# Performance work log

Hardware: AMD Instinct MI355X
Metric: run time of the kernel (lower is better)

Reference implementation:

```python
import jax, jax.numpy as jnp
import numpy as np

N = 50_000          # num_nodes
E = 800_000         # num_edges (avg degree 16)
DIMS = [512, 256, 256, 7]   # embedding_dim
SCALING = 2.0


def _glorot(key, shape):
    lim = float(np.sqrt(6.0 / (shape[0] + shape[1])))
    return jax.random.uniform(key, shape, jnp.float32, -lim, lim)


def setup_inputs() -> dict:
    key = jax.random.key(0)
    ks = jax.random.split(key, 16)
    inp = {
        "x": jax.random.normal(ks[0], (N, DIMS[0]), jnp.float32),
        "edge_index": jax.random.randint(ks[1], (2, E), 0, N, dtype=jnp.int32),
        # GCNConv weights (3 layers)
        "W1": _glorot(ks[2], (DIMS[0], DIMS[1])), "b1": jnp.zeros((DIMS[1],), jnp.float32),
        "W2": _glorot(ks[3], (DIMS[1], DIMS[2])), "b2": jnp.zeros((DIMS[2],), jnp.float32),
        "W3": _glorot(ks[4], (DIMS[2], DIMS[3])), "b3": jnp.zeros((DIMS[3],), jnp.float32),
        # pseudo_mlp: Linear(512,512) -> ReLU -> Linear(512,64) -> ReLU -> Linear(64,out)
        "mw1": _glorot(ks[5], (DIMS[0], 512)), "mb1": jnp.zeros((512,), jnp.float32),
        "mw2": _glorot(ks[6], (512, 64)),      "mb2": jnp.zeros((64,), jnp.float32),
        "mw3": _glorot(ks[7], (64, DIMS[-1])), "mb3": jnp.zeros((DIMS[-1],), jnp.float32),
        # parsing_mats[0] (only index 0 is used: learn_soft_edge3 always called with ln=0)
        "parsing0": jnp.ones((DIMS[-1], DIMS[-1]), jnp.float32) / SCALING,
    }
    return inp


def _gcn_conv(h_in, row, col, edge_weight, W, b):
    """PyG-style GCNConv with self-loops, symmetric norm, and per-edge weights."""
    h = h_in @ W                                  # [N, out]
    loop = jnp.arange(N, dtype=row.dtype)
    r = jnp.concatenate([row, loop])
    c = jnp.concatenate([col, loop])
    ew = jnp.concatenate([edge_weight, jnp.ones((N,), h.dtype)])
    deg = jax.ops.segment_sum(ew, c, num_segments=N)
    dinv = jnp.where(deg > 0, jax.lax.rsqrt(jnp.maximum(deg, 1e-12)), 0.0)
    norm = dinv[r] * ew * dinv[c]                 # [E+N]
    out = jax.ops.segment_sum(h[r] * norm[:, None], c, num_segments=N)
    return out + b


def _learn_soft_edge(x, row, col, mw1, mb1, mw2, mb2, mw3, mb3, parsing0):
    # pseudo_mlp logits
    h = jax.nn.relu(x @ mw1 + mb1)
    h = jax.nn.relu(h @ mw2 + mb2)
    logits = h @ mw3 + mb3                        # [N, C]
    s = logits[row]                               # start_logits [E, C]
    e = logits[col]                               # end_logits   [E, C]
    parsing = jax.nn.relu(SCALING * parsing0)     # [C, C]
    # diag(bmm(outer(s,e), P)).sum(-1) == sum_{c,d} s[e,c] * e[e,d] * P[d,c]
    ew = jnp.sum(s * (e @ parsing), axis=1)       # [E]
    mean = ew.mean()
    var = ew.var(ddof=1)                          # torch .var() is unbiased
    return (ew - mean) * jnp.sqrt(1e-4 / var) + 1.0


def reference(x, edge_index, W1, b1, W2, b2, W3, b3,
              mw1, mb1, mw2, mb2, mw3, mb3, parsing0):
    row, col = edge_index[0], edge_index[1]
    ew = _learn_soft_edge(x, row, col, mw1, mb1, mw2, mb2, mw3, mb3, parsing0)
    # layer 0
    h0 = _gcn_conv(x, row, col, ew, W1, b1)       # h = x (saved, pre-ReLU)
    x1 = jax.nn.relu(h0)                          # dropout is identity in eval
    # layer 1 (+ residual to h0)
    x2 = _gcn_conv(x1, row, col, ew, W2, b2)
    x2 = jax.nn.relu(x2) + h0
    # layer 2 (final, no activation)
    out = _gcn_conv(x2, row, col, ew, W3, b3)     # [N, n_classes]
    return out
```

## Files before the change

### kernel.cpp

```cpp
#include <hip/hip_runtime.h>

#define NN 50000
#define EE 800000
#define NB_EDGE 3125
#define NB_E1   1563
#define NB_SCAN 196

typedef __attribute__((ext_vector_type(4))) float f32x4;
typedef __attribute__((ext_vector_type(8))) short bf16x8;
typedef __attribute__((ext_vector_type(8))) unsigned short u16x8;

typedef const __attribute__((address_space(1))) void* gas_p;
typedef __attribute__((address_space(3))) void* las_p;

__device__ __forceinline__ float bf2f(unsigned short u) {
  union { unsigned int i; float f; } v; v.i = ((unsigned int)u) << 16; return v.f;
}
__device__ __forceinline__ unsigned short f2bf(float f) {
  union { float f; unsigned int i; } v; v.f = f;
  unsigned int u = v.i;
  return (unsigned short)((u + 0x7FFFu + ((u >> 16) & 1u)) >> 16);
}

__device__ __forceinline__ int xcd_swizzle(int orig, int nwg) {
  int xcd = orig & 7;
  int pos = orig >> 3;
  int q = nwg >> 3, r = nwg & 7;
  return (xcd < r ? xcd * (q + 1) : r * (q + 1) + (xcd - r) * q) + pos;
}

constexpr size_t O_XBF  = 0;
constexpr size_t O_H1   = O_XBF + 51200000;
constexpr size_t O_G1   = O_H1  + 51200000;
constexpr size_t O_X1   = O_G1  + 25600000;
constexpr size_t O_H2   = O_X1  + 25600000;
constexpr size_t O_LG   = O_H2  + 6400000;
constexpr size_t O_TG   = O_LG  + 1600000;
constexpr size_t O_EWR  = O_TG  + 1600000;
constexpr size_t O_W3P  = O_EWR + 3200000;
constexpr size_t O_CSR  = O_W3P + 3200000;
constexpr size_t O_MW1T = O_CSR + 6400000;
constexpr size_t O_W1T  = O_MW1T + 524288;
constexpr size_t O_W2T  = O_W1T  + 262144;
constexpr size_t O_MW2T = O_W2T  + 131072;
constexpr size_t O_DEG  = O_MW2T + 65536;
constexpr size_t O_CNT  = O_DEG  + 200192;
constexpr size_t O_CUR  = O_CNT  + 200192;
constexpr size_t O_RED  = O_CUR  + 200192;
constexpr size_t O_RPT  = O_RED  + 256;
constexpr size_t O_DINV = O_RPT  + 200192;
constexpr size_t O_BSUM = O_DINV + 200192;

__global__ __launch_bounds__(256) void conv_f2bf4(const float* __restrict__ in,
                                                  unsigned short* __restrict__ out, int n4) {
  int i = blockIdx.x * 256 + threadIdx.x;
  if (i >= n4) return;
  const float4 v = ((const float4*)in)[i];
  ushort4 o; o.x = f2bf(v.x); o.y = f2bf(v.y); o.z = f2bf(v.z); o.w = f2bf(v.w);
  ((ushort4*)out)[i] = o;
}

__global__ __launch_bounds__(256)
void conv_weights(const float* __restrict__ mw1, const float* __restrict__ W1,
                  const float* __restrict__ W2, const float* __restrict__ mw2,
                  const float* __restrict__ W3,
                  unsigned short* __restrict__ mw1t, unsigned short* __restrict__ w1t,
                  unsigned short* __restrict__ w2t, unsigned short* __restrict__ mw2t,
                  float* __restrict__ w3p)
{
  int i = blockIdx.x * 256 + threadIdx.x;
  if (i < 262144) {
    int k = i >> 9, n = i & 511;
    mw1t[(size_t)n * 512 + k] = f2bf(mw1[i]);
  } else if (i < 393216) {
    int j = i - 262144, k = j >> 8, n = j & 255;
    w1t[(size_t)n * 512 + k] = f2bf(W1[j]);
  } else if (i < 458752) {
    int j = i - 393216, k = j >> 8, n = j & 255;
    w2t[(size_t)n * 256 + k] = f2bf(W2[j]);
  } else if (i < 491520) {
    int j = i - 458752, k = j >> 6, n = j & 63;
    mw2t[(size_t)n * 512 + k] = f2bf(mw2[j]);
  } else if (i < 493568) {
    int j = i - 491520, d = j >> 3, c = j & 7;
    w3p[j] = (c < 7) ? W3[d * 7 + c] : 0.f;
  }
}

#define GEMM_STAGE(buf, k0)                                                        \
  _Pragma("unroll")                                                                \
  for (int r = 0; r < 4; ++r) {                                                    \
    const int row = r * 32 + wid * 8 + srow8;                                      \
    int ga = bm + row; ga = ga < M_ ? ga : M_ - 1;                                 \
    int gb = bn + row; gb = gb < N_ ? gb : N_ - 1;                                 \
    __builtin_amdgcn_global_load_lds((gas_p)(pA_ + ((size_t)ga * lda_ + (k0)) * 2 + sks * 16), \
                                     (las_p)(ldsA[buf] + row * 64), 16, 0, 0);     \
    __builtin_amdgcn_global_load_lds((gas_p)(pB_ + ((size_t)gb * ldb_ + (k0)) * 2 + sks * 16), \
                                     (las_p)(ldsB[buf] + row * 64), 16, 0, 0);     \
  }

#define GEMM_BODY(A, lda, Bt, ldb_K, M, Ncols, K, bm, bn)                          \
  __shared__ unsigned short ldsA[2][128 * 64];                                     \
  __shared__ unsigned short ldsB[2][128 * 64];                                     \
  const char* pA_ = (const char*)(A);                                              \
  const char* pB_ = (const char*)(Bt);                                             \
  const int lda_ = (lda), ldb_ = (ldb_K), M_ = (M), N_ = (Ncols);                  \
  const int tid  = threadIdx.x;                                                    \
  const int lane = tid & 63;                                                       \
  const int wid  = tid >> 6;                                                       \
  const int wm   = (wid >> 1) << 6;                                                \
  const int wn   = (wid & 1) << 6;                                                 \
  f32x4 acc[4][4] = {};                                                            \
  const int srow8 = lane >> 3;                                                     \
  const int sks   = (lane & 7) ^ srow8;                                            \
  const int nt    = (K) >> 6;                                                      \
  GEMM_STAGE(0, 0)                                                                 \
  for (int t = 0; t < nt; ++t) {                                                   \
    const int cur = t & 1;                                                         \
    if (t + 1 < nt) {                                                              \
      GEMM_STAGE(cur ^ 1, (t + 1) << 6)                                            \
      asm volatile("s_waitcnt vmcnt(8)" ::: "memory");                             \
    } else {                                                                       \
      asm volatile("s_waitcnt vmcnt(0)" ::: "memory");                             \
    }                                                                              \
    __builtin_amdgcn_s_barrier();                                                  \
    __builtin_amdgcn_sched_barrier(0);                                             \
    const int q   = lane >> 4;                                                     \
    const int r15 = lane & 15;                                                     \
    _Pragma("unroll")                                                              \
    for (int kk = 0; kk < 2; ++kk) {                                               \
      bf16x8 af[4], bfr[4];                                                        \
      _Pragma("unroll")                                                            \
      for (int m = 0; m < 4; ++m) {                                                \
        const int ra = wm + m * 16 + r15;                                          \
        af[m]  = *(const bf16x8*)(ldsA[cur] + ra * 64 + (((kk << 2) + q) ^ (ra & 7)) * 8); \
        const int rb = wn + m * 16 + r15;                                          \
        bfr[m] = *(const bf16x8*)(ldsB[cur] + rb * 64 + (((kk << 2) + q) ^ (rb & 7)) * 8); \
      }                                                                            \
      _Pragma("unroll")                                                            \
      for (int m = 0; m < 4; ++m)                                                  \
        _Pragma("unroll")                                                          \
        for (int n = 0; n < 4; ++n)                                                \
          acc[m][n] = __builtin_amdgcn_mfma_f32_16x16x32_bf16(af[m], bfr[n], acc[m][n], 0, 0, 0); \
    }                                                                              \
    __builtin_amdgcn_sched_barrier(0);                                             \
    __builtin_amdgcn_s_barrier();                                                  \
  }

template<bool RELU, bool BIAS>
__global__ __launch_bounds__(256)
void gemm_bf16(const unsigned short* __restrict__ A, int lda,
               const unsigned short* __restrict__ Bt,
               const float* __restrict__ bias,
               unsigned short* __restrict__ C, int ldc,
               int M, int N, int K)
{
  const int nwg  = gridDim.x * gridDim.y;
  const int wgid = xcd_swizzle(blockIdx.y * gridDim.x + blockIdx.x, nwg);
  const int bn   = (wgid % gridDim.x) << 7;
  const int bm   = (wgid / gridDim.x) << 7;

  GEMM_BODY(A, lda, Bt, K, M, N, K, bm, bn)

  const int q   = lane >> 4;
  const int r15 = lane & 15;
#pragma unroll
  for (int m = 0; m < 4; ++m) {
#pragma unroll
    for (int n = 0; n < 4; ++n) {
      const int gc = bn + wn + n * 16 + r15;
#pragma unroll
      for (int i = 0; i < 4; ++i) {
        const int gr = bm + wm + m * 16 + q * 4 + i;
        if (gr < M && gc < N) {
          float f = acc[m][n][i];
          if (BIAS) f += bias[gc];
          if (RELU) f = fmaxf(f, 0.f);
          C[(size_t)gr * ldc + gc] = f2bf(f);
        }
      }
    }
  }
}

__global__ __launch_bounds__(256)
void gemm_fused(const unsigned short* __restrict__ A,
                const unsigned short* __restrict__ Bt,
                const float* __restrict__ mb1,
                unsigned short* __restrict__ h1,
                unsigned short* __restrict__ g1,
                int M)
{
  const int nwg  = gridDim.x * gridDim.y;
  const int wgid = xcd_swizzle(blockIdx.y * gridDim.x + blockIdx.x, nwg);
  const int bnt  = wgid % gridDim.x;
  const int bn   = bnt << 7;
  const int bm   = (wgid / gridDim.x) << 7;

  GEMM_BODY(A, 512, Bt, 512, M, 768, 512, bm, bn)

  const int q   = lane >> 4;
  const int r15 = lane & 15;
  if (bnt < 4) {
#pragma unroll
    for (int m = 0; m < 4; ++m) {
#pragma unroll
      for (int n = 0; n < 4; ++n) {
        const int gc = bn + wn + n * 16 + r15;
        const float b = mb1[gc];
#pragma unroll
        for (int i = 0; i < 4; ++i) {
          const int gr = bm + wm + m * 16 + q * 4 + i;
          if (gr < M) h1[(size_t)gr * 512 + gc] = f2bf(fmaxf(acc[m][n][i] + b, 0.f));
        }
      }
    }
  } else {
#pragma unroll
    for (int m = 0; m < 4; ++m) {
#pragma unroll
      for (int n = 0; n < 4; ++n) {
        const int gc = bn - 512 + wn + n * 16 + r15;
#pragma unroll
        for (int i = 0; i < 4; ++i) {
          const int gr = bm + wm + m * 16 + q * 4 + i;
          if (gr < M) g1[(size_t)gr * 256 + gc] = f2bf(acc[m][n][i]);
        }
      }
    }
  }
}

__global__ __launch_bounds__(256)
void logits_kernel(const unsigned short* __restrict__ h2, const float* __restrict__ mw3,
                   const float* __restrict__ mb3, const float* __restrict__ par,
                   float* __restrict__ Lg, float* __restrict__ Tg)
{
  __shared__ float w[64 * 8];
  __shared__ float P[64];
  int tid = threadIdx.x;
  for (int i = tid; i < 512; i += 256) {
    int k = i >> 3, c = i & 7;
    w[i] = (c < 7) ? mw3[k * 7 + c] : 0.f;
  }
  if (tid < 64) {
    int d = tid >> 3, c = tid & 7;
    P[tid] = (d < 7 && c < 7) ? fmaxf(2.0f * par[d * 7 + c], 0.f) : 0.f;
  }
  __syncthreads();
  int n = blockIdx.x * 256 + tid;
  if (n >= NN) return;
  const unsigned short* hr = h2 + (size_t)n * 64;
  f32x4 L0 = {0,0,0,0}, L1 = {0,0,0,0};
  for (int k = 0; k < 64; k += 4) {
    ushort4 v = *(const ushort4*)(hr + k);
    float xs[4] = {bf2f(v.x), bf2f(v.y), bf2f(v.z), bf2f(v.w)};
#pragma unroll
    for (int j = 0; j < 4; ++j) {
      L0 += xs[j] * *(const f32x4*)&w[(k + j) * 8];
      L1 += xs[j] * *(const f32x4*)&w[(k + j) * 8 + 4];
    }
  }
  float Ls[8] = {L0[0], L0[1], L0[2], L0[3], L1[0], L1[1], L1[2], 0.f};
#pragma unroll
  for (int c = 0; c < 7; ++c) Ls[c] += mb3[c];
  f32x4 T0 = {0,0,0,0}, T1 = {0,0,0,0};
#pragma unroll
  for (int d = 0; d < 7; ++d) {
    T0 += Ls[d] * *(const f32x4*)&P[d * 8];
    T1 += Ls[d] * *(const f32x4*)&P[d * 8 + 4];
  }
  f32x4 o0 = {Ls[0], Ls[1], Ls[2], Ls[3]};
  f32x4 o1 = {Ls[4], Ls[5], Ls[6], 0.f};
  *(f32x4*)(Lg + (size_t)n * 8)     = o0;
  *(f32x4*)(Lg + (size_t)n * 8 + 4) = o1;
  *(f32x4*)(Tg + (size_t)n * 8)     = T0;
  *(f32x4*)(Tg + (size_t)n * 8 + 4) = T1;
}

__global__ __launch_bounds__(256)
void edge1_kernel(const int* __restrict__ row, const int* __restrict__ col,
                  const float* __restrict__ Lg, const float* __restrict__ Tg,
                  float* __restrict__ ew_raw, int* __restrict__ cnt,
                  double* __restrict__ part)
{
  __shared__ double shs[4], shs2[4];
  const int e0 = blockIdx.x * 512 + threadIdx.x;
  const int e1 = e0 + 256;
  double s = 0.0, s2 = 0.0;
  if (e1 < EE) {
    int r0 = row[e0], c0 = col[e0];
    int r1 = row[e1], c1 = col[e1];
    float4 a00 = *(const float4*)(Lg + (size_t)r0 * 8);
    float4 a01 = *(const float4*)(Lg + (size_t)r0 * 8 + 4);
    float4 a10 = *(const float4*)(Lg + (size_t)r1 * 8);
    float4 a11 = *(const float4*)(Lg + (size_t)r1 * 8 + 4);
    float4 b00 = *(const float4*)(Tg + (size_t)c0 * 8);
    float4 b01 = *(const float4*)(Tg + (size_t)c0 * 8 + 4);
    float4 b10 = *(const float4*)(Tg + (size_t)c1 * 8);
    float4 b11 = *(const float4*)(Tg + (size_t)c1 * 8 + 4);
    float v0 = a00.x*b00.x + a00.y*b00.y + a00.z*b00.z + a00.w*b00.w
             + a01.x*b01.x + a01.y*b01.y + a01.z*b01.z + a01.w*b01.w;
    float v1 = a10.x*b10.x + a10.y*b10.y + a10.z*b10.z + a10.w*b10.w
             + a11.x*b11.x + a11.y*b11.y + a11.z*b11.z + a11.w*b11.w;
    ew_raw[e0] = v0; ew_raw[e1] = v1;
    atomicAdd(&cnt[c0], 1); atomicAdd(&cnt[c1], 1);
    s = (double)v0 + (double)v1;
    s2 = (double)v0 * (double)v0 + (double)v1 * (double)v1;
  } else if (e0 < EE) {
    int r0 = row[e0], c0 = col[e0];
    float4 a00 = *(const float4*)(Lg + (size_t)r0 * 8);
    float4 a01 = *(const float4*)(Lg + (size_t)r0 * 8 + 4);
    float4 b00 = *(const float4*)(Tg + (size_t)c0 * 8);
    float4 b01 = *(const float4*)(Tg + (size_t)c0 * 8 + 4);
    float v0 = a00.x*b00.x + a00.y*b00.y + a00.z*b00.z + a00.w*b00.w
             + a01.x*b01.x + a01.y*b01.y + a01.z*b01.z + a01.w*b01.w;
    ew_raw[e0] = v0;
    atomicAdd(&cnt[c0], 1);
    s = (double)v0; s2 = (double)v0 * (double)v0;
  }
  for (int off = 32; off; off >>= 1) {
    s  += __shfl_down(s, off);
    s2 += __shfl_down(s2, off);
  }
  int wv = threadIdx.x >> 6;
  if ((threadIdx.x & 63) == 0) { shs[wv] = s; shs2[wv] = s2; }
  __syncthreads();
  if (threadIdx.x == 0) {
    part[blockIdx.x]         = shs[0] + shs[1] + shs[2] + shs[3];
    part[NB_E1 + blockIdx.x] = shs2[0] + shs2[1] + shs2[2] + shs2[3];
  }
}

__global__ __launch_bounds__(1024)
void redpart_kernel(const double* __restrict__ part, double* __restrict__ red)
{
  __shared__ double sh[16][2];
  int tid = threadIdx.x;
  double s = 0.0, s2 = 0.0;
  for (int i = tid; i < NB_E1; i += 1024) {
    s  += part[i];
    s2 += part[NB_E1 + i];
  }
  for (int off = 32; off; off >>= 1) {
    s  += __shfl_down(s, off);
    s2 += __shfl_down(s2, off);
  }
  if ((tid & 63) == 0) { sh[tid >> 6][0] = s; sh[tid >> 6][1] = s2; }
  __syncthreads();
  if (tid == 0) {
    double a = 0.0, b = 0.0;
    for (int i = 0; i < 16; ++i) { a += sh[i][0]; b += sh[i][1]; }
    red[0] = a; red[1] = b;
  }
}

__global__ __launch_bounds__(256)
void edge2_kernel(const int* __restrict__ row, const int* __restrict__ col,
                  const float* __restrict__ ew_raw, const double* __restrict__ red,
                  const int* __restrict__ rowptr, int* __restrict__ cursor,
                  float* __restrict__ deg, int2* __restrict__ csr_sw)
{
  int e = blockIdx.x * 256 + threadIdx.x;
  if (e >= EE) return;
  double mean = red[0] / (double)EE;
  double var  = (red[1] - (double)EE * mean * mean) / (double)(EE - 1);
  double scl  = sqrt(1e-4 / var);
  float v = (float)(((double)ew_raw[e] - mean) * scl) + 1.0f;
  int c = col[e];
  atomicAdd(&deg[c], v);
  int pos = atomicAdd(&cursor[c], 1);
  int2 sw; sw.x = row[e]; sw.y = __float_as_int(v);
  csr_sw[rowptr[c] + pos] = sw;
}

__global__ __launch_bounds__(256)
void dinv_kernel(const float* __restrict__ deg, float* __restrict__ dinv)
{
  int n = blockIdx.x * 256 + threadIdx.x;
  if (n >= NN) return;
  float d = deg[n] + 1.0f;
  dinv[n] = d > 0.f ? 1.0f / sqrtf(fmaxf(d, 1e-12f)) : 0.f;
}

__global__ __launch_bounds__(256)
void scale_csr_kernel(int2* __restrict__ csr_sw, const float* __restrict__ dinv)
{
  int i = blockIdx.x * 256 + threadIdx.x;
  if (i >= EE) return;
  int2 sw = csr_sw[i];
  sw.y = __float_as_int(__int_as_float(sw.y) * dinv[sw.x]);
  csr_sw[i] = sw;
}

__global__ __launch_bounds__(256)
void scan1_kernel(const int* __restrict__ cnt, int* __restrict__ bsum)
{
  __shared__ int sh[4];
  int i = blockIdx.x * 256 + threadIdx.x;
  int v = (i < NN) ? cnt[i] : 0;
  for (int off = 32; off; off >>= 1) v += __shfl_down(v, off);
  if ((threadIdx.x & 63) == 0) sh[threadIdx.x >> 6] = v;
  __syncthreads();
  if (threadIdx.x == 0) bsum[blockIdx.x] = sh[0] + sh[1] + sh[2] + sh[3];
}

__global__ __launch_bounds__(256)
void scan2_kernel(int* __restrict__ bsum)
{
  __shared__ int sh[256];
  int tid = threadIdx.x;
  int v = (tid < NB_SCAN) ? bsum[tid] : 0;
  sh[tid] = v;
  __syncthreads();
  for (int off = 1; off < 256; off <<= 1) {
    int t = (tid >= off) ? sh[tid - off] : 0;
    __syncthreads();
    sh[tid] += t;
    __syncthreads();
  }
  if (tid < NB_SCAN) bsum[tid] = sh[tid] - v;
}

__global__ __launch_bounds__(256)
void scan3_kernel(const int* __restrict__ cnt, const int* __restrict__ bsum,
                  int* __restrict__ rowptr)
{
  __shared__ int sh[256];
  int tid = threadIdx.x;
  int i = blockIdx.x * 256 + tid;
  int v = (i < NN) ? cnt[i] : 0;
  sh[tid] = v;
  __syncthreads();
  for (int off = 1; off < 256; off <<= 1) {
    int t = (tid >= off) ? sh[tid - off] : 0;
    __syncthreads();
    sh[tid] += t;
    __syncthreads();
  }
  if (i < NN) rowptr[i + 1] = bsum[blockIdx.x] + sh[tid];
  if (i == 0) rowptr[0] = 0;
}

#define AGG_ACC(sw_, v_)                                                     \
  {                                                                          \
    float w_ = __int_as_float((sw_).y);                                      \
    a0 += w_ * bf2f((v_)[0]); a1 += w_ * bf2f((v_)[1]);                      \
    a2 += w_ * bf2f((v_)[2]); a3 += w_ * bf2f((v_)[3]);                      \
    a4 += w_ * bf2f((v_)[4]); a5 += w_ * bf2f((v_)[5]);                      \
    a6 += w_ * bf2f((v_)[6]); a7 += w_ * bf2f((v_)[7]);                      \
  }

template<int MODE>
__global__ __launch_bounds__(256)
void agg256_kernel(const int* __restrict__ rowptr, const int2* __restrict__ csr_sw,
                   const unsigned short* __restrict__ gsrc,
                   const float* __restrict__ dinv, const float* __restrict__ bias,
                   const unsigned short* __restrict__ h0in,
                   unsigned short* __restrict__ h0out,
                   unsigned short* __restrict__ xout,
                   const float* __restrict__ w3p, float* __restrict__ y3)
{
  const int tid = threadIdx.x;
  const int hw  = tid >> 5;
  const int l5  = tid & 31;
  const size_t colbase = (size_t)(l5 << 3);
  const int stride = (int)gridDim.x * 8;

  for (int n = blockIdx.x * 8 + hw; n < NN; n += stride) {
    float a0=0,a1=0,a2=0,a3=0,a4=0,a5=0,a6=0,a7=0;
    const int s = rowptr[n], e = rowptr[n + 1];
    int i = s;
    for (; i + 7 < e; i += 8) {
      int2 sw[8];
#pragma unroll
      for (int u = 0; u < 8; ++u) sw[u] = csr_sw[i + u];
      u16x8 v[8];
#pragma unroll
      for (int u = 0; u < 8; ++u) v[u] = *(const u16x8*)(gsrc + (size_t)sw[u].x * 256 + colbase);
#pragma unroll
      for (int u = 0; u < 8; ++u) AGG_ACC(sw[u], v[u])
    }
    for (; i + 3 < e; i += 4) {
      int2 sw[4];
#pragma unroll
      for (int u = 0; u < 4; ++u) sw[u] = csr_sw[i + u];
      u16x8 v[4];
#pragma unroll
      for (int u = 0; u < 4; ++u) v[u] = *(const u16x8*)(gsrc + (size_t)sw[u].x * 256 + colbase);
#pragma unroll
      for (int u = 0; u < 4; ++u) AGG_ACC(sw[u], v[u])
    }
    for (; i < e; ++i) {
      int2 sw = csr_sw[i];
      u16x8 v = *(const u16x8*)(gsrc + (size_t)sw.x * 256 + colbase);
      AGG_ACC(sw, v)
    }
    const int dbase = l5 << 3;
    const float dn = dinv[n];
    const float wd = dn * dn;
    u16x8 sv = *(const u16x8*)(gsrc + (size_t)n * 256 + dbase);
    float4 b0 = *(const float4*)(bias + dbase);
    float4 b1 = *(const float4*)(bias + dbase + 4);
    float f0 = dn * a0 + wd * bf2f(sv[0]) + b0.x;
    float f1 = dn * a1 + wd * bf2f(sv[1]) + b0.y;
    float f2 = dn * a2 + wd * bf2f(sv[2]) + b0.z;
    float f3 = dn * a3 + wd * bf2f(sv[3]) + b0.w;
    float f4 = dn * a4 + wd * bf2f(sv[4]) + b1.x;
    float f5 = dn * a5 + wd * bf2f(sv[5]) + b1.y;
    float f6 = dn * a6 + wd * bf2f(sv[6]) + b1.z;
    float f7 = dn * a7 + wd * bf2f(sv[7]) + b1.w;
    const size_t o = (size_t)n * 256 + dbase;
    if (MODE == 0) {
      u16x8 h;
      h[0] = f2bf(f0); h[1] = f2bf(f1); h[2] = f2bf(f2); h[3] = f2bf(f3);
      h[4] = f2bf(f4); h[5] = f2bf(f5); h[6] = f2bf(f6); h[7] = f2bf(f7);
      *(u16x8*)(h0out + o) = h;
      u16x8 xo;
      xo[0] = f2bf(fmaxf(f0, 0.f)); xo[1] = f2bf(fmaxf(f1, 0.f));
      xo[2] = f2bf(fmaxf(f2, 0.f)); xo[3] = f2bf(fmaxf(f3, 0.f));
      xo[4] = f2bf(fmaxf(f4, 0.f)); xo[5] = f2bf(fmaxf(f5, 0.f));
      xo[6] = f2bf(fmaxf(f6, 0.f)); xo[7] = f2bf(fmaxf(f7, 0.f));
      *(u16x8*)(xout + o) = xo;
    } else {
      u16x8 h = *(const u16x8*)(h0in + o);
      float xv0 = bf2f(f2bf(fmaxf(f0, 0.f) + bf2f(h[0])));
      float xv1 = bf2f(f2bf(fmaxf(f1, 0.f) + bf2f(h[1])));
      float xv2 = bf2f(f2bf(fmaxf(f2, 0.f) + bf2f(h[2])));
      float xv3 = bf2f(f2bf(fmaxf(f3, 0.f) + bf2f(h[3])));
      float xv4 = bf2f(f2bf(fmaxf(f4, 0.f) + bf2f(h[4])));
      float xv5 = bf2f(f2bf(fmaxf(f5, 0.f) + bf2f(h[5])));
      float xv6 = bf2f(f2bf(fmaxf(f6, 0.f) + bf2f(h[6])));
      float xv7 = bf2f(f2bf(fmaxf(f7, 0.f) + bf2f(h[7])));
      const float* w3r = w3p + (size_t)dbase * 8;
      f32x4 p0 = {0,0,0,0}, p1 = {0,0,0,0};
      p0 += xv0 * *(const f32x4*)(w3r +  0); p1 += xv0 * *(const f32x4*)(w3r +  4);
      p0 += xv1 * *(const f32x4*)(w3r +  8); p1 += xv1 * *(const f32x4*)(w3r + 12);
      p0 += xv2 * *(const f32x4*)(w3r + 16); p1 += xv2 * *(const f32x4*)(w3r + 20);
      p0 += xv3 * *(const f32x4*)(w3r + 24); p1 += xv3 * *(const f32x4*)(w3r + 28);
      p0 += xv4 * *(const f32x4*)(w3r + 32); p1 += xv4 * *(const f32x4*)(w3r + 36);
      p0 += xv5 * *(const f32x4*)(w3r + 40); p1 += xv5 * *(const f32x4*)(w3r + 44);
      p0 += xv6 * *(const f32x4*)(w3r + 48); p1 += xv6 * *(const f32x4*)(w3r + 52);
      p0 += xv7 * *(const f32x4*)(w3r + 56); p1 += xv7 * *(const f32x4*)(w3r + 60);
#pragma unroll
      for (int off = 1; off < 32; off <<= 1) {
        p0[0] += __shfl_xor(p0[0], off); p0[1] += __shfl_xor(p0[1], off);
        p0[2] += __shfl_xor(p0[2], off); p0[3] += __shfl_xor(p0[3], off);
        p1[0] += __shfl_xor(p1[0], off); p1[1] += __shfl_xor(p1[1], off);
        p1[2] += __shfl_xor(p1[2], off); p1[3] += __shfl_xor(p1[3], off);
      }
      if (l5 == 0) {
        *(f32x4*)(y3 + (size_t)n * 8)     = p0;
        *(f32x4*)(y3 + (size_t)n * 8 + 4) = p1;
      }
    }
  }
}

__global__ __launch_bounds__(256)
void agg7_kernel(const int* __restrict__ rowptr, const int2* __restrict__ csr_sw,
                 const float* __restrict__ y3,
                 const float* __restrict__ dinv, const float* __restrict__ b3,
                 float* __restrict__ out)
{
  int n = blockIdx.x * 32 + (threadIdx.x >> 3);
  if (n >= NN) return;
  int j = threadIdx.x & 7;
  float acc = 0.f;
  int s = rowptr[n], e = rowptr[n + 1];
  for (int i = s; i < e; ++i) {
    int2 sw = csr_sw[i];
    acc += __int_as_float(sw.y) * y3[(size_t)sw.x * 8 + j];
  }
  float dn = dinv[n];
  acc = dn * acc + dn * dn * y3[(size_t)n * 8 + j];
  if (j < 7) out[(size_t)n * 7 + j] = acc + b3[j];
}

extern "C" void kernel_launch(void* const* d_in, const int* in_sizes, int n_in,
                              void* d_out, int out_size, void* d_ws, size_t ws_size,
                              hipStream_t stream)
{
  const float* x   = (const float*)d_in[0];
  const int*   ei  = (const int*)d_in[1];
  const float* W1  = (const float*)d_in[2];
  const float* b1  = (const float*)d_in[3];
  const float* W2  = (const float*)d_in[4];
  const float* b2  = (const float*)d_in[5];
  const float* W3  = (const float*)d_in[6];
  const float* b3  = (const float*)d_in[7];
  const float* mw1 = (const float*)d_in[8];
  const float* mb1 = (const float*)d_in[9];
  const float* mw2 = (const float*)d_in[10];
  const float* mb2 = (const float*)d_in[11];
  const float* mw3 = (const float*)d_in[12];
  const float* mb3 = (const float*)d_in[13];
  const float* par = (const float*)d_in[14];
  const int* row = ei;
  const int* col = ei + EE;
  float* out = (float*)d_out;

  char* ws = (char*)d_ws;
  unsigned short* x_bf  = (unsigned short*)(ws + O_XBF);
  unsigned short* h0    = (unsigned short*)(ws + O_XBF);
  unsigned short* h1_bf = (unsigned short*)(ws + O_H1);
  unsigned short* g2_bf = (unsigned short*)(ws + O_H1);
  unsigned short* g1_bf = (unsigned short*)(ws + O_G1);
  unsigned short* x1_bf = (unsigned short*)(ws + O_X1);
  unsigned short* h2_bf = (unsigned short*)(ws + O_H2);
  float* Lg      = (float*)(ws + O_LG);
  float* Tg      = (float*)(ws + O_TG);
  float* ew_raw  = (float*)(ws + O_EWR);
  float* y3      = (float*)(ws + O_EWR);
  float* w3p     = (float*)(ws + O_W3P);
  int2*  csr_sw  = (int2*)(ws + O_CSR);
  double* part   = (double*)(ws + O_CSR);
  unsigned short* mw1t = (unsigned short*)(ws + O_MW1T);
  unsigned short* w1t  = (unsigned short*)(ws + O_W1T);
  unsigned short* w2t  = (unsigned short*)(ws + O_W2T);
  unsigned short* mw2t = (unsigned short*)(ws + O_MW2T);
  float*  deg    = (float*)(ws + O_DEG);
  int*    cnt    = (int*)(ws + O_CNT);
  int*    cursor = (int*)(ws + O_CUR);
  double* red    = (double*)(ws + O_RED);
  int*    rowptr = (int*)(ws + O_RPT);
  float*  dinv   = (float*)(ws + O_DINV);
  int*    bsum   = (int*)(ws + O_BSUM);

  hipMemsetAsync(ws + O_DEG, 0, 3 * 200192, stream);

  conv_f2bf4<<<25000, 256, 0, stream>>>(x, x_bf, NN * 512 / 4);
  conv_weights<<<1929, 256, 0, stream>>>(mw1, W1, W2, mw2, W3, mw1t, w1t, w2t, mw2t, w3p);

  gemm_fused<<<dim3(6, 391), 256, 0, stream>>>(x_bf, mw1t, mb1, h1_bf, g1_bf, NN);
  gemm_bf16<true,  true ><<<dim3(1, 391), 256, 0, stream>>>(h1_bf, 512, mw2t, mb2, h2_bf, 64, NN, 64, 512);
  logits_kernel<<<196, 256, 0, stream>>>(h2_bf, mw3, mb3, par, Lg, Tg);

  edge1_kernel<<<NB_E1, 256, 0, stream>>>(row, col, Lg, Tg, ew_raw, cnt, part);
  redpart_kernel<<<1, 1024, 0, stream>>>(part, red);
  scan1_kernel<<<NB_SCAN, 256, 0, stream>>>(cnt, bsum);
  scan2_kernel<<<1, 256, 0, stream>>>(bsum);
  scan3_kernel<<<NB_SCAN, 256, 0, stream>>>(cnt, bsum, rowptr);
  edge2_kernel<<<NB_EDGE, 256, 0, stream>>>(row, col, ew_raw, red, rowptr, cursor, deg, csr_sw);
  dinv_kernel<<<196, 256, 0, stream>>>(deg, dinv);
  scale_csr_kernel<<<NB_EDGE, 256, 0, stream>>>(csr_sw, dinv);

  agg256_kernel<0><<<2048, 256, 0, stream>>>(rowptr, csr_sw, g1_bf, dinv, b1, nullptr, h0, x1_bf, nullptr, nullptr);
  gemm_bf16<false, false><<<dim3(2, 391), 256, 0, stream>>>(x1_bf, 256, w2t, nullptr, g2_bf, 256, NN, 256, 256);
  agg256_kernel<1><<<2048, 256, 0, stream>>>(rowptr, csr_sw, g2_bf, dinv, b2, h0, nullptr, nullptr, w3p, y3);
  agg7_kernel<<<1563, 256, 0, stream>>>(rowptr, csr_sw, y3, dinv, b3, out);
}
```

Measured before the change: 441.8 us.

## Compute degrees from raw edge sums and fold normalization into CSR build

Degree is now derived algebraically from per-node raw edge-weight sums and counts gathered in edge1, so dinv is computed before CSR construction. edge2 writes the dinv-scaled weight directly, which removes the separate scale_csr pass and the float degree atomics in edge2. The change also adds launch bounds with an occupancy hint and fewer blocks for agg256, and unrolls the agg7 gather loop by four. It adds one float atomic per edge in edge1, and computing the degree as a sum of raw values followed by scaling could change rounding slightly.

New measurement: 506.4 us. +14.6%, slower.

```diff
diff --git a/kernel.cpp b/kernel.cpp
--- a/kernel.cpp
+++ b/kernel.cpp
@@ -43,8 +43,8 @@
 constexpr size_t O_W1T  = O_MW1T + 524288;
 constexpr size_t O_W2T  = O_W1T  + 262144;
 constexpr size_t O_MW2T = O_W2T  + 131072;
-constexpr size_t O_DEG  = O_MW2T + 65536;
-constexpr size_t O_CNT  = O_DEG  + 200192;
+constexpr size_t O_SRAW = O_MW2T + 65536;
+constexpr size_t O_CNT  = O_SRAW + 200192;
 constexpr size_t O_CUR  = O_CNT  + 200192;
 constexpr size_t O_RED  = O_CUR  + 200192;
 constexpr size_t O_RPT  = O_RED  + 256;
@@ -282,7 +282,7 @@
 void edge1_kernel(const int* __restrict__ row, const int* __restrict__ col,
                   const float* __restrict__ Lg, const float* __restrict__ Tg,
                   float* __restrict__ ew_raw, int* __restrict__ cnt,
-                  double* __restrict__ part)
+                  float* __restrict__ sraw, double* __restrict__ part)
 {
   __shared__ double shs[4], shs2[4];
   const int e0 = blockIdx.x * 512 + threadIdx.x;
@@ -305,6 +305,7 @@
              + a11.x*b11.x + a11.y*b11.y + a11.z*b11.z + a11.w*b11.w;
     ew_raw[e0] = v0; ew_raw[e1] = v1;
     atomicAdd(&cnt[c0], 1); atomicAdd(&cnt[c1], 1);
+    atomicAdd(&sraw[c0], v0); atomicAdd(&sraw[c1], v1);
     s = (double)v0 + (double)v1;
     s2 = (double)v0 * (double)v0 + (double)v1 * (double)v1;
   } else if (e0 < EE) {
@@ -317,6 +318,7 @@
              + a01.x*b01.x + a01.y*b01.y + a01.z*b01.z + a01.w*b01.w;
     ew_raw[e0] = v0;
     atomicAdd(&cnt[c0], 1);
+    atomicAdd(&sraw[c0], v0);
     s = (double)v0; s2 = (double)v0 * (double)v0;
   }
   for (int off = 32; off; off >>= 1) {
@@ -356,10 +358,25 @@
 }
 
 __global__ __launch_bounds__(256)
+void dinv_kernel(const float* __restrict__ sraw, const int* __restrict__ cnt,
+                 const double* __restrict__ red, float* __restrict__ dinv)
+{
+  int n = blockIdx.x * 256 + threadIdx.x;
+  if (n >= NN) return;
+  double mean = red[0] / (double)EE;
+  double var  = (red[1] - (double)EE * mean * mean) / (double)(EE - 1);
+  double scl  = sqrt(1e-4 / var);
+  double c    = (double)cnt[n];
+  double deg  = scl * ((double)sraw[n] - c * mean) + c;
+  float d = (float)deg + 1.0f;
+  dinv[n] = d > 0.f ? 1.0f / sqrtf(fmaxf(d, 1e-12f)) : 0.f;
+}
+
+__global__ __launch_bounds__(256)
 void edge2_kernel(const int* __restrict__ row, const int* __restrict__ col,
                   const float* __restrict__ ew_raw, const double* __restrict__ red,
                   const int* __restrict__ rowptr, int* __restrict__ cursor,
-                  float* __restrict__ deg, int2* __restrict__ csr_sw)
+                  const float* __restrict__ dinv, int2* __restrict__ csr_sw)
 {
   int e = blockIdx.x * 256 + threadIdx.x;
   if (e >= EE) return;
@@ -367,30 +384,11 @@
   double var  = (red[1] - (double)EE * mean * mean) / (double)(EE - 1);
   double scl  = sqrt(1e-4 / var);
   float v = (float)(((double)ew_raw[e] - mean) * scl) + 1.0f;
-  int c = col[e];
-  atomicAdd(&deg[c], v);
+  int r = row[e], c = col[e];
+  float w = v * dinv[r];
   int pos = atomicAdd(&cursor[c], 1);
-  int2 sw; sw.x = row[e]; sw.y = __float_as_int(v);
+  int2 sw; sw.x = r; sw.y = __float_as_int(w);
   csr_sw[rowptr[c] + pos] = sw;
-}
-
-__global__ __launch_bounds__(256)
-void dinv_kernel(const float* __restrict__ deg, float* __restrict__ dinv)
-{
-  int n = blockIdx.x * 256 + threadIdx.x;
-  if (n >= NN) return;
-  float d = deg[n] + 1.0f;
-  dinv[n] = d > 0.f ? 1.0f / sqrtf(fmaxf(d, 1e-12f)) : 0.f;
-}
-
-__global__ __launch_bounds__(256)
-void scale_csr_kernel(int2* __restrict__ csr_sw, const float* __restrict__ dinv)
-{
-  int i = blockIdx.x * 256 + threadIdx.x;
-  if (i >= EE) return;
-  int2 sw = csr_sw[i];
-  sw.y = __float_as_int(__int_as_float(sw.y) * dinv[sw.x]);
-  csr_sw[i] = sw;
 }
 
 __global__ __launch_bounds__(256)
@@ -452,7 +450,7 @@
   }
 
 template<int MODE>
-__global__ __launch_bounds__(256)
+__global__ __launch_bounds__(256, 6)
 void agg256_kernel(const int* __restrict__ rowptr, const int2* __restrict__ csr_sw,
                    const unsigned short* __restrict__ gsrc,
                    const float* __restrict__ dinv, const float* __restrict__ bias,
@@ -568,7 +566,18 @@
   int j = threadIdx.x & 7;
   float acc = 0.f;
   int s = rowptr[n], e = rowptr[n + 1];
-  for (int i = s; i < e; ++i) {
+  int i = s;
+  for (; i + 3 < e; i += 4) {
+    int2 sw0 = csr_sw[i],     sw1 = csr_sw[i + 1];
+    int2 sw2 = csr_sw[i + 2], sw3 = csr_sw[i + 3];
+    float v0 = y3[(size_t)sw0.x * 8 + j];
+    float v1 = y3[(size_t)sw1.x * 8 + j];
+    float v2 = y3[(size_t)sw2.x * 8 + j];
+    float v3 = y3[(size_t)sw3.x * 8 + j];
+    acc += __int_as_float(sw0.y) * v0 + __int_as_float(sw1.y) * v1
+         + __int_as_float(sw2.y) * v2 + __int_as_float(sw3.y) * v3;
+  }
+  for (; i < e; ++i) {
     int2 sw = csr_sw[i];
     acc += __int_as_float(sw.y) * y3[(size_t)sw.x * 8 + j];
   }
@@ -619,7 +628,7 @@
   unsigned short* w1t  = (unsigned short*)(ws + O_W1T);
   unsigned short* w2t  = (unsigned short*)(ws + O_W2T);
   unsigned short* mw2t = (unsigned short*)(ws + O_MW2T);
-  float*  deg    = (float*)(ws + O_DEG);
+  float*  sraw   = (float*)(ws + O_SRAW);
   int*    cnt    = (int*)(ws + O_CNT);
   int*    cursor = (int*)(ws + O_CUR);
   double* red    = (double*)(ws + O_RED);
@@ -627,7 +636,7 @@
   float*  dinv   = (float*)(ws + O_DINV);
   int*    bsum   = (int*)(ws + O_BSUM);
 
-  hipMemsetAsync(ws + O_DEG, 0, 3 * 200192, stream);
+  hipMemsetAsync(ws + O_SRAW, 0, 3 * 200192, stream);
 
   conv_f2bf4<<<25000, 256, 0, stream>>>(x, x_bf, NN * 512 / 4);
   conv_weights<<<1929, 256, 0, stream>>>(mw1, W1, W2, mw2, W3, mw1t, w1t, w2t, mw2t, w3p);
@@ -636,17 +645,16 @@
   gemm_bf16<true,  true ><<<dim3(1, 391), 256, 0, stream>>>(h1_bf, 512, mw2t, mb2, h2_bf, 64, NN, 64, 512);
   logits_kernel<<<196, 256, 0, stream>>>(h2_bf, mw3, mb3, par, Lg, Tg);
 
-  edge1_kernel<<<NB_E1, 256, 0, stream>>>(row, col, Lg, Tg, ew_raw, cnt, part);
+  edge1_kernel<<<NB_E1, 256, 0, stream>>>(row, col, Lg, Tg, ew_raw, cnt, sraw, part);
   redpart_kernel<<<1, 1024, 0, stream>>>(part, red);
   scan1_kernel<<<NB_SCAN, 256, 0, stream>>>(cnt, bsum);
   scan2_kernel<<<1, 256, 0, stream>>>(bsum);
   scan3_kernel<<<NB_SCAN, 256, 0, stream>>>(cnt, bsum, rowptr);
-  edge2_kernel<<<NB_EDGE, 256, 0, stream>>>(row, col, ew_raw, red, rowptr, cursor, deg, csr_sw);
-  dinv_kernel<<<196, 256, 0, stream>>>(deg, dinv);
-  scale_csr_kernel<<<NB_EDGE, 256, 0, stream>>>(csr_sw, dinv);
-
-  agg256_kernel<0><<<2048, 256, 0, stream>>>(rowptr, csr_sw, g1_bf, dinv, b1, nullptr, h0, x1_bf, nullptr, nullptr);
+  dinv_kernel<<<196, 256, 0, stream>>>(sraw, cnt, red, dinv);
+  edge2_kernel<<<NB_EDGE, 256, 0, stream>>>(row, col, ew_raw, red, rowptr, cursor, dinv, csr_sw);
+
+  agg256_kernel<0><<<1536, 256, 0, stream>>>(rowptr, csr_sw, g1_bf, dinv, b1, nullptr, h0, x1_bf, nullptr, nullptr);
   gemm_bf16<false, false><<<dim3(2, 391), 256, 0, stream>>>(x1_bf, 256, w2t, nullptr, g2_bf, 256, NN, 256, 256);
-  agg256_kernel<1><<<2048, 256, 0, stream>>>(rowptr, csr_sw, g2_bf, dinv, b2, h0, nullptr, nullptr, w3p, y3);
+  agg256_kernel<1><<<1536, 256, 0, stream>>>(rowptr, csr_sw, g2_bf, dinv, b2, h0, nullptr, nullptr, w3p, y3);
   agg7_kernel<<<1563, 256, 0, stream>>>(rowptr, csr_sw, y3, dinv, b3, out);
 }
```
